# Performance work log

Hardware: AMD Instinct MI355X
Metric: run time of the kernel (lower is better)

## Reference

```python
import jax, jax.numpy as jnp
import numpy as np

B = 8192       # batch (tokens)
D = 2048       # data_dim
DEPTH = 3      # tree depth: 1 root + 2 mid + 4 leaf experts
INIT = 0.02


def setup_inputs() -> dict:
    key = jax.random.key(0)
    ks = jax.random.split(key, 6)
    x = jax.random.normal(ks[0], (B, D), dtype=jnp.float32)
    # router output simulated as i.i.d. path bits (router is a frozen pretrained black box)
    path_mask = jax.random.randint(ks[1], (B, DEPTH), 0, 2, dtype=jnp.int32)
    W0 = jax.random.normal(ks[2], (D, D), dtype=jnp.float32) * INIT
    b0 = jnp.zeros((D,), dtype=jnp.float32)
    W1 = jax.random.normal(ks[3], (2, D, D), dtype=jnp.float32) * INIT  # depth-1 experts
    b1 = jnp.zeros((2, D), dtype=jnp.float32)
    W2 = jax.random.normal(ks[4], (4, D, D), dtype=jnp.float32) * INIT  # depth-2 (leaf) experts
    b2 = jnp.zeros((4, D), dtype=jnp.float32)
    return {"x": x, "W0": W0, "b0": b0, "W1": W1, "b1": b1,
            "W2": W2, "b2": b2, "path_mask": path_mask}


def reference(x, W0, b0, W1, b1, W2, b2, path_mask):
    # Root expert (depth 0): applied to all tokens.
    h0 = jax.nn.relu(x @ W0 + b0)                                  # [B, D]
    bit0 = path_mask[:, 0]                                          # routes depth-1 children
    bit1 = path_mask[:, 1]                                          # routes depth-2 children
    # Depth-1: 2 experts; dense compute then per-token select (static-shape MoE dispatch).
    h1_all = jax.nn.relu(jnp.einsum('bd,edf->bef', h0, W1) + b1)    # [B, 2, D]
    h1 = jnp.take_along_axis(h1_all, bit0[:, None, None].astype(jnp.int32), axis=1)[:, 0]
    # Depth-2 (leaves): 4 experts indexed by the 2-bit path.
    leaf = 2 * bit0 + bit1                                          # [B] in {0,1,2,3}
    h2_all = jax.nn.relu(jnp.einsum('bd,edf->bef', h1, W2) + b2)    # [B, 4, D]
    y = jnp.take_along_axis(h2_all, leaf[:, None, None].astype(jnp.int32), axis=1)[:, 0]
    return y
```

## Files before the change

### kernel.cpp

```cpp
#include <hip/hip_runtime.h>

#define BB 8192
#define DD 2048
#define NSLOT 7
#define NP1 (BB + 2*128)
#define NP2 (BB + 4*128)

typedef unsigned short u16;
typedef unsigned int   u32;
typedef unsigned long long u64;

typedef __bf16 bf16x8 __attribute__((ext_vector_type(8)));
typedef float  f32x4  __attribute__((ext_vector_type(4)));

#define OFF_WT   0ull
#define OFF_XB   (OFF_WT + (size_t)NSLOT*DD*DD*2)
#define OFF_H0   (OFF_XB + (size_t)BB*DD*2)
#define OFF_P1   (OFF_H0 + (size_t)BB*DD*2)
#define OFF_P2   (OFF_P1 + (size_t)NP1*4)
#define OFF_META (OFF_P2 + (size_t)NP2*4)

__device__ __forceinline__ u16 f2bf(float f) {
  u32 u = __float_as_uint(f);
  u32 r = (u + 0x7FFFu + ((u >> 16) & 1u)) >> 16;
  return (u16)r;
}
__device__ __forceinline__ float bf2f(u16 u) {
  return __uint_as_float(((u32)u) << 16);
}

__device__ __forceinline__ void gld16(const void* g, void* l) {
  __builtin_amdgcn_global_load_lds(
      (const __attribute__((address_space(1))) void*)g,
      (__attribute__((address_space(3))) void*)l, 16, 0, 0);
}


__global__ void k_detect(const u16* x, int* meta) {
  __shared__ int cnt, cntz;
  if (threadIdx.x == 0) { cnt = 0; cntz = 0; }
  __syncthreads();
  u16 u = x[threadIdx.x * 17];
  int ex = (u >> 7) & 0xFF;
  int sane = (ex == 0) || (ex >= 112 && ex <= 143);
  atomicAdd(&cnt, sane);
  atomicAdd(&cntz, (u == 0) ? 1 : 0);
  __syncthreads();
  if (threadIdx.x == 0) meta[20] = (cnt >= 205 && cntz < 64) ? 1 : 0;
}

__global__ __launch_bounds__(1024) void k_route(const int* __restrict__ pm,
                                                int* __restrict__ p1,
                                                int* __restrict__ p2,
                                                int* __restrict__ meta) {
  __shared__ int cnt[6];
  __shared__ int cur[6];
  __shared__ int base1[2], base2[4];
  const int tid = threadIdx.x;
  const int lane = tid & 63;
  if (tid < 6) { cnt[tid] = 0; cur[tid] = 0; }
  __syncthreads();

  for (int i = tid; i < NP1; i += 1024) p1[i] = -1;
  for (int i = tid; i < NP2; i += 1024) p2[i] = -1;

  int myb0[8], myleaf[8];
  #pragma unroll
  for (int i = 0; i < 8; ++i) {
    int b = i * 1024 + tid;
    int b0 = pm[b*3] & 1, b1 = pm[b*3+1] & 1;
    myb0[i] = b0; myleaf[i] = b0*2 + b1;
  }
  #pragma unroll
  for (int i = 0; i < 8; ++i) {
    u64 m0 = __ballot(myb0[i] == 0);
    if (lane == 0) {
      atomicAdd(&cnt[0], __popcll(m0));
      atomicAdd(&cnt[1], 64 - __popcll(m0));
    }
    #pragma unroll
    for (int e = 0; e < 4; ++e) {
      u64 me = __ballot(myleaf[i] == e);
      if (lane == 0) atomicAdd(&cnt[2+e], __popcll(me));
    }
  }
  __syncthreads();
  if (tid == 0) {
    base1[0] = 0;
    base1[1] = (cnt[0] + 127) & ~127;
    meta[12] = 0; meta[13] = base1[1];
    meta[14] = base1[1] + ((cnt[1] + 127) & ~127);
    int b = 0;
    #pragma unroll
    for (int e = 0; e < 4; ++e) {
      base2[e] = b; meta[15+e] = b;
      b += (cnt[2+e] + 127) & ~127;
    }
    meta[19] = b;
  }
  __syncthreads();
  #pragma unroll
  for (int i = 0; i < 8; ++i) {
    int b = i * 1024 + tid;
    u64 lt = (1ull << lane) - 1ull;
    #pragma unroll
    for (int g = 0; g < 2; ++g) {
      u64 m = __ballot(myb0[i] == g);
      int pos = __popcll(m & lt);
      int wbase = 0;
      if (lane == 0 && m) wbase = atomicAdd(&cur[g], __popcll(m));
      wbase = __shfl(wbase, 0);
      if (myb0[i] == g) p1[base1[g] + wbase + pos] = b;
    }
    #pragma unroll
    for (int g = 0; g < 4; ++g) {
      u64 m = __ballot(myleaf[i] == g);
      int pos = __popcll(m & lt);
      int wbase = 0;
      if (lane == 0 && m) wbase = atomicAdd(&cur[2+g], __popcll(m));
      wbase = __shfl(wbase, 0);
      if (myleaf[i] == g) p2[base2[g] + wbase + pos] = b;
    }
  }
}

__global__ void k_cvtx(const void* __restrict__ x, u16* __restrict__ xb,
                       const int* __restrict__ meta) {
  int i = blockIdx.x * 256 + threadIdx.x;
  if (meta[20]) {
    ((uint4*)xb)[i] = ((const uint4*)x)[i];
  } else {
    const float4* p = (const float4*)x + (size_t)i * 2;
    float4 a = p[0], b = p[1];
    uint4 o;
    o.x = f2bf(a.x) | ((u32)f2bf(a.y) << 16);
    o.y = f2bf(a.z) | ((u32)f2bf(a.w) << 16);
    o.z = f2bf(b.x) | ((u32)f2bf(b.y) << 16);
    o.w = f2bf(b.z) | ((u32)f2bf(b.w) << 16);
    ((uint4*)xb)[i] = o;
  }
}

__global__ void k_wt(const void* __restrict__ W0, const void* __restrict__ W1,
                     const void* __restrict__ W2, u16* __restrict__ wt,
                     const int* __restrict__ meta) {
  __shared__ float tile[64][65];
  int bid = blockIdx.x;
  int slot = bid >> 10;
  int t = bid & 1023;
  int tr = t >> 5, tc = t & 31;
  const void* src; size_t eoff;
  if (slot == 0)      { src = W0; eoff = 0; }
  else if (slot <= 2) { src = W1; eoff = (size_t)(slot-1)*DD*DD; }
  else                { src = W2; eoff = (size_t)(slot-3)*DD*DD; }
  int r0 = tr*64, c0 = tc*64;
  int tid = threadIdx.x;
  int isbf = meta[20];
  #pragma unroll
  for (int i = 0; i < 4; ++i) {
    int idx = tid + i*256;
    int r = idx >> 4, c4 = (idx & 15) * 4;
    size_t goff = eoff + (size_t)(r0 + r)*DD + c0 + c4;
    if (isbf) {
      ushort4 v = *(const ushort4*)((const u16*)src + goff);
      tile[r][c4+0] = bf2f(v.x); tile[r][c4+1] = bf2f(v.y);
      tile[r][c4+2] = bf2f(v.z); tile[r][c4+3] = bf2f(v.w);
    } else {
      float4 v = *(const float4*)((const float*)src + goff);
      tile[r][c4+0] = v.x; tile[r][c4+1] = v.y;
      tile[r][c4+2] = v.z; tile[r][c4+3] = v.w;
    }
  }
  __syncthreads();
  u16* dst = wt + (size_t)slot*DD*DD;
  #pragma unroll
  for (int i = 0; i < 4; ++i) {
    int idx = tid + i*256;
    int orow = idx >> 4, oc = (idx & 15) * 4;
    uint2 o;
    o.x = f2bf(tile[oc+0][orow]) | ((u32)f2bf(tile[oc+1][orow]) << 16);
    o.y = f2bf(tile[oc+2][orow]) | ((u32)f2bf(tile[oc+3][orow]) << 16);
    *(uint2*)&dst[(size_t)(c0 + orow)*DD + r0 + oc] = o;
  }
}

__global__ __launch_bounds__(256, 2) void k_gemm(
    const u16* __restrict__ A, const u16* __restrict__ Wt,
    const void* __restrict__ bias, const int* __restrict__ perm,
    const int* __restrict__ bases, int nexp,
    void* __restrict__ Out, int final_out, const int* __restrict__ meta) {
  __shared__ __align__(16) u16 As[128*32];
  __shared__ __align__(16) u16 Bs[128*32];

  const int tid  = threadIdx.x;
  const int wid  = tid >> 6;
  const int lane = tid & 63;
  const int m0 = blockIdx.x * 128;
  const int n0 = blockIdx.y * 128;

  int e = 0;
  if (nexp == 2)      e = (m0 >= bases[1]);
  else if (nexp == 4) e = (m0 >= bases[1]) + (m0 >= bases[2]) + (m0 >= bases[3]);
  const u16* W = Wt + (size_t)e * DD * DD;

  const u16* gA[2]; const u16* gB[2];
  u16* lA[2]; u16* lB[2];
  #pragma unroll
  for (int p = 0; p < 2; ++p) {
    int seg  = p*4 + wid;
    int boff = seg*1024 + lane*16;
    int row  = boff >> 6;
    int kk   = (boff & 63) >> 1;
    int gr = m0 + row;
    if (perm) { int t = perm[gr]; gr = (t < 0) ? 0 : t; }
    gA[p] = A + (size_t)gr * DD + kk;
    gB[p] = W + (size_t)(n0 + row) * DD + kk;
    lA[p] = (u16*)((char*)As + seg*1024);
    lB[p] = (u16*)((char*)Bs + seg*1024);
  }

  f32x4 zero = {0.0f, 0.0f, 0.0f, 0.0f};
  f32x4 acc[4][4];
  #pragma unroll
  for (int i = 0; i < 4; ++i)
    #pragma unroll
    for (int j = 0; j < 4; ++j) acc[i][j] = zero;

  const int wm = wid & 1, wn = wid >> 1;
  const int q = lane >> 4, cl = lane & 15;
  const int aoff = (wm*64 + cl) * 32 + q*8;
  const int boff2 = (wn*64 + cl) * 32 + q*8;

  for (int k0 = 0; k0 < DD; k0 += 32) {
    gld16(gA[0] + k0, lA[0]);
    gld16(gA[1] + k0, lA[1]);
    gld16(gB[0] + k0, lB[0]);
    gld16(gB[1] + k0, lB[1]);
    __syncthreads();
    bf16x8 af[4], bf[4];
    #pragma unroll
    for (int mt = 0; mt < 4; ++mt) af[mt] = *(const bf16x8*)&As[aoff + mt*16*32];
    #pragma unroll
    for (int nt = 0; nt < 4; ++nt) bf[nt] = *(const bf16x8*)&Bs[boff2 + nt*16*32];
    #pragma unroll
    for (int mt = 0; mt < 4; ++mt)
      #pragma unroll
      for (int nt = 0; nt < 4; ++nt)
        acc[mt][nt] = __builtin_amdgcn_mfma_f32_16x16x32_bf16(af[mt], bf[nt], acc[mt][nt], 0, 0, 0);
    __syncthreads();
  }

  const int isbf = meta[20];
  float bv[4];
  #pragma unroll
  for (int nt = 0; nt < 4; ++nt) {
    int col = n0 + wn*64 + nt*16 + cl;
    bv[nt] = isbf ? bf2f(((const u16*)bias)[e*DD + col])
                  : ((const float*)bias)[e*DD + col];
  }
  #pragma unroll
  for (int mt = 0; mt < 4; ++mt) {
    int rbase = m0 + wm*64 + mt*16 + q*4;
    #pragma unroll
    for (int r = 0; r < 4; ++r) {
      int row = rbase + r;
      int orow = row;
      if (perm) { orow = perm[row]; if (orow < 0) continue; }
      #pragma unroll
      for (int nt = 0; nt < 4; ++nt) {
        int col = n0 + wn*64 + nt*16 + cl;
        float v = acc[mt][nt][r] + bv[nt];
        v = v > 0.0f ? v : 0.0f;
        if (!final_out || isbf) ((u16*)Out)[(size_t)orow*DD + col] = f2bf(v);
        else                    ((float*)Out)[(size_t)orow*DD + col] = v;
      }
    }
  }
}

extern "C" void kernel_launch(void* const* d_in, const int* in_sizes, int n_in,
                              void* d_out, int out_size, void* d_ws, size_t ws_size,
                              hipStream_t stream) {
  (void)in_sizes; (void)n_in; (void)out_size; (void)ws_size;
  const void* x  = d_in[0];
  const void* W0 = d_in[1];
  const void* b0 = d_in[2];
  const void* W1 = d_in[3];
  const void* b1 = d_in[4];
  const void* W2 = d_in[5];
  const void* b2 = d_in[6];
  const int*  pm = (const int*)d_in[7];

  char* ws  = (char*)d_ws;
  u16*  wt  = (u16*)(ws + OFF_WT);
  u16*  xb  = (u16*)(ws + OFF_XB);
  u16*  h0  = (u16*)(ws + OFF_H0);
  u16*  h1  = xb;
  int*  p1  = (int*)(ws + OFF_P1);
  int*  p2  = (int*)(ws + OFF_P2);
  int*  meta= (int*)(ws + OFF_META);

  hipLaunchKernelGGL(k_detect, dim3(1),  dim3(256),  0, stream, (const u16*)x, meta);
  hipLaunchKernelGGL(k_route,  dim3(1),  dim3(1024), 0, stream, pm, p1, p2, meta);
  hipLaunchKernelGGL(k_cvtx,   dim3(BB*DD/8/256), dim3(256), 0, stream, x, xb, meta);
  hipLaunchKernelGGL(k_wt,     dim3(7*1024), dim3(256), 0, stream, W0, W1, W2, wt, meta);

  hipLaunchKernelGGL(k_gemm, dim3(64, 16), dim3(256), 0, stream,
                     xb, wt, b0, (const int*)nullptr, (const int*)nullptr, 1,
                     (void*)h0, 0, meta);
  hipLaunchKernelGGL(k_gemm, dim3(66, 16), dim3(256), 0, stream,
                     h0, wt + (size_t)1*DD*DD, b1, p1, meta + 12, 2,
                     (void*)h1, 0, meta);
  hipLaunchKernelGGL(k_gemm, dim3(68, 16), dim3(256), 0, stream,
                     h1, wt + (size_t)3*DD*DD, b2, p2, meta + 15, 4,
                     d_out, 1, meta);
}
```

Before: 568.1 us.

## Swizzle GEMM LDS layout, swap grid order, and store weight transpose tile as bf16

```diff
diff --git a/kernel.cpp b/kernel.cpp
--- a/kernel.cpp
+++ b/kernel.cpp
@@ -12,6 +12,7 @@
 
 typedef __bf16 bf16x8 __attribute__((ext_vector_type(8)));
 typedef float  f32x4  __attribute__((ext_vector_type(4)));
+typedef u16    u16x8  __attribute__((ext_vector_type(8)));
 
 #define OFF_WT   0ull
 #define OFF_XB   (OFF_WT + (size_t)NSLOT*DD*DD*2)
@@ -144,7 +145,7 @@
 __global__ void k_wt(const void* __restrict__ W0, const void* __restrict__ W1,
                      const void* __restrict__ W2, u16* __restrict__ wt,
                      const int* __restrict__ meta) {
-  __shared__ float tile[64][65];
+  __shared__ u16 tile[64][66];
   int bid = blockIdx.x;
   int slot = bid >> 10;
   int t = bid & 1023;
@@ -161,26 +162,27 @@
     int idx = tid + i*256;
     int r = idx >> 4, c4 = (idx & 15) * 4;
     size_t goff = eoff + (size_t)(r0 + r)*DD + c0 + c4;
+    u16 v0, v1, v2, v3;
     if (isbf) {
       ushort4 v = *(const ushort4*)((const u16*)src + goff);
-      tile[r][c4+0] = bf2f(v.x); tile[r][c4+1] = bf2f(v.y);
-      tile[r][c4+2] = bf2f(v.z); tile[r][c4+3] = bf2f(v.w);
+      v0 = v.x; v1 = v.y; v2 = v.z; v3 = v.w;
     } else {
       float4 v = *(const float4*)((const float*)src + goff);
-      tile[r][c4+0] = v.x; tile[r][c4+1] = v.y;
-      tile[r][c4+2] = v.z; tile[r][c4+3] = v.w;
-    }
+      v0 = f2bf(v.x); v1 = f2bf(v.y); v2 = f2bf(v.z); v3 = f2bf(v.w);
+    }
+    tile[r][c4+0] = v0; tile[r][c4+1] = v1;
+    tile[r][c4+2] = v2; tile[r][c4+3] = v3;
   }
   __syncthreads();
   u16* dst = wt + (size_t)slot*DD*DD;
   #pragma unroll
-  for (int i = 0; i < 4; ++i) {
+  for (int i = 0; i < 2; ++i) {
     int idx = tid + i*256;
-    int orow = idx >> 4, oc = (idx & 15) * 4;
-    uint2 o;
-    o.x = f2bf(tile[oc+0][orow]) | ((u32)f2bf(tile[oc+1][orow]) << 16);
-    o.y = f2bf(tile[oc+2][orow]) | ((u32)f2bf(tile[oc+3][orow]) << 16);
-    *(uint2*)&dst[(size_t)(c0 + orow)*DD + r0 + oc] = o;
+    int n = idx >> 3, j = idx & 7;
+    u16x8 o;
+    #pragma unroll
+    for (int k = 0; k < 8; ++k) o[k] = tile[j*8 + k][n];
+    *(u16x8*)&dst[(size_t)(c0 + n)*DD + r0 + j*8] = o;
   }
 }
 
@@ -195,8 +197,8 @@
   const int tid  = threadIdx.x;
   const int wid  = tid >> 6;
   const int lane = tid & 63;
-  const int m0 = blockIdx.x * 128;
-  const int n0 = blockIdx.y * 128;
+  const int m0 = blockIdx.y * 128;
+  const int n0 = blockIdx.x * 128;
 
   int e = 0;
   if (nexp == 2)      e = (m0 >= bases[1]);
@@ -207,10 +209,11 @@
   u16* lA[2]; u16* lB[2];
   #pragma unroll
   for (int p = 0; p < 2; ++p) {
-    int seg  = p*4 + wid;
-    int boff = seg*1024 + lane*16;
-    int row  = boff >> 6;
-    int kk   = (boff & 63) >> 1;
+    int seg   = p*4 + wid;
+    int boff  = seg*1024 + lane*16;
+    int row   = boff >> 6;
+    int chunk = (boff >> 4) & 3;
+    int kk    = (chunk ^ ((row >> 1) & 3)) * 8;
     int gr = m0 + row;
     if (perm) { int t = perm[gr]; gr = (t < 0) ? 0 : t; }
     gA[p] = A + (size_t)gr * DD + kk;
@@ -228,8 +231,9 @@
 
   const int wm = wid & 1, wn = wid >> 1;
   const int q = lane >> 4, cl = lane & 15;
-  const int aoff = (wm*64 + cl) * 32 + q*8;
-  const int boff2 = (wn*64 + cl) * 32 + q*8;
+  const int sw = q ^ ((cl >> 1) & 3);
+  const int aoff  = (wm*64 + cl) * 32 + sw*8;
+  const int boff2 = (wn*64 + cl) * 32 + sw*8;
 
   for (int k0 = 0; k0 < DD; k0 += 32) {
     gld16(gA[0] + k0, lA[0]);
@@ -305,13 +309,13 @@
   hipLaunchKernelGGL(k_cvtx,   dim3(BB*DD/8/256), dim3(256), 0, stream, x, xb, meta);
   hipLaunchKernelGGL(k_wt,     dim3(7*1024), dim3(256), 0, stream, W0, W1, W2, wt, meta);
 
-  hipLaunchKernelGGL(k_gemm, dim3(64, 16), dim3(256), 0, stream,
+  hipLaunchKernelGGL(k_gemm, dim3(16, 64), dim3(256), 0, stream,
                      xb, wt, b0, (const int*)nullptr, (const int*)nullptr, 1,
                      (void*)h0, 0, meta);
-  hipLaunchKernelGGL(k_gemm, dim3(66, 16), dim3(256), 0, stream,
+  hipLaunchKernelGGL(k_gemm, dim3(16, 66), dim3(256), 0, stream,
                      h0, wt + (size_t)1*DD*DD, b1, p1, meta + 12, 2,
                      (void*)h1, 0, meta);
-  hipLaunchKernelGGL(k_gemm, dim3(68, 16), dim3(256), 0, stream,
+  hipLaunchKernelGGL(k_gemm, dim3(16, 68), dim3(256), 0, stream,
                      h1, wt + (size_t)3*DD*DD, b2, p2, meta + 15, 4,
                      d_out, 1, meta);
 }
```

New measurement: 540.8 us. 1.05x faster.
